# Kernel optimization log

Hardware: AMD Instinct MI355X
Metric: run time of the kernel (lower is better)

## Reference

```python
import jax, jax.numpy as jnp
import numpy as np

NEG_BIG = 1.0e10


def _strict_causal_mask(n):
    # mask[i, j] = 1.0 for j < i (strictly lower triangular), matching the
    # original loop `causal_mask[i, :i] = 1.0`.
    return jnp.tril(jnp.ones((n, n), dtype=jnp.float32), k=-1)


def setup_inputs() -> dict:
    rng = jax.random.key(0)
    k1, k2, k3 = jax.random.split(rng, 3)
    B, C, H, W = 8, 128, 64, 64
    return {
        "key": jax.random.normal(k1, (B, C, H, W), dtype=jnp.float32),
        "mixin": jax.random.normal(k2, (B, C, H, W), dtype=jnp.float32),
        "query": jax.random.normal(k3, (B, C, H, W), dtype=jnp.float32),
    }


def reference(key, mixin, query):
    B, Cq, H, W = query.shape
    Ck = key.shape[1]
    Cm = mixin.shape[1]
    N = H * W  # canvas_size

    # [B, C, H, W] -> [B, N, C]
    q = query.transpose(0, 2, 3, 1).reshape(B, N, Cq)
    k = key.transpose(0, 2, 3, 1).reshape(B, N, Ck)
    m = mixin.transpose(0, 2, 3, 1).reshape(B, N, Cm)

    mask = _strict_causal_mask(N)  # [N, N], broadcast over batch

    # raw scores with large-constant masking (matches original order of ops)
    dot = jnp.einsum("bqc,bkc->bqk", q, k) - (1.0 - mask) * NEG_BIG
    # NOTE: original subtracts the row max BEFORE scaling by 1/sqrt(d)
    dot = dot - jnp.max(dot, axis=-1, keepdims=True)
    causal_exp = jnp.exp(dot / jnp.sqrt(jnp.float32(Ck))) * mask
    probs = causal_exp / (jnp.sum(causal_exp, axis=-1, keepdims=True) + 1e-6)

    mixed = jnp.einsum("bqk,bkc->bqc", probs, m)  # [B, N, Cm]
    return mixed.reshape(B, H, W, Cm).transpose(0, 3, 1, 2)
```

## Files before the change

### kernel.cpp

```cpp
#include <hip/hip_runtime.h>
#include <hip/hip_bf16.h>
#include <stdint.h>


#define BATCH 8
#define CH    128
#define NN    4096
#define QBLK  64
#define KVBLK 64
#define C2 0.12751745f

typedef __attribute__((ext_vector_type(8))) short short8;
typedef __attribute__((ext_vector_type(16))) float f32x16;
typedef __attribute__((ext_vector_type(2))) int v2i;

__device__ __forceinline__ void gload16(const void* g, void* l) {
  __builtin_amdgcn_global_load_lds(
      (const __attribute__((address_space(1))) void*)g,
      (__attribute__((address_space(3))) void*)l, 16, 0, 0);
}

__device__ __forceinline__ int pk_bf16(float lo, float hi) {
  int d;
  asm("v_cvt_pk_bf16_f32 %0, %1, %2" : "=v"(d) : "v"(lo), "v"(hi));
  return d;
}

__device__ __forceinline__ void plswap(int& a, int& b) {
  v2i r = __builtin_amdgcn_permlane32_swap(a, b, false, false);
  a = r[0]; b = r[1];
}

__global__ __launch_bounds__(256) void prep_kernel(
    const float* __restrict__ key, const float* __restrict__ mixin,
    const float* __restrict__ query,
    unsigned short* __restrict__ qt, unsigned short* __restrict__ kt,
    unsigned short* __restrict__ vb) {
  int bid = blockIdx.x;
  int t = threadIdx.x;
  if (bid < 8192) {
    __shared__ float tl[32][33];
    const float* src = (bid < 4096) ? query : key;
    unsigned short* dst = (bid < 4096) ? qt : kt;
    int id = bid & 4095;
    int b = id >> 9;
    int tile = id & 511;
    int n0 = (tile >> 2) << 5;
    int c0 = (tile & 3) << 5;
    const float* sb = src + (size_t)b * CH * NN;
#pragma unroll
    for (int it = 0; it < 4; ++it) {
      int cl = it * 8 + (t >> 5);
      int nl = t & 31;
      tl[cl][nl] = sb[(size_t)(c0 + cl) * NN + n0 + nl];
    }
    __syncthreads();
    int nl = t >> 3;
    int cq = (t & 7) * 4;
    int d0 = pk_bf16(tl[cq + 0][nl], tl[cq + 1][nl]);
    int d1 = pk_bf16(tl[cq + 2][nl], tl[cq + 3][nl]);
    *(v2i*)&dst[(size_t)(b * NN + n0 + nl) * CH + c0 + cq] = (v2i){d0, d1};
  } else {
    int id = bid - 8192;
    size_t base = (size_t)id * 4096 + t * 4;
#pragma unroll
    for (int it = 0; it < 4; ++it) {
      size_t idx = base + (size_t)it * 1024;
      float4 v = *(const float4*)&mixin[idx];
      int d0 = pk_bf16(v.x, v.y);
      int d1 = pk_bf16(v.z, v.w);
      *(v2i*)&vb[idx] = (v2i){d0, d1};
    }
  }
}

__global__ __launch_bounds__(256, 2) void attn_kernel(
    const unsigned short* __restrict__ qt, const unsigned short* __restrict__ kt,
    const unsigned short* __restrict__ vb, float* __restrict__ out) {
  __shared__ __align__(16) unsigned char smem[65536];
  int tid = threadIdx.x;
  int wid = tid >> 6;
  int lane = tid & 63;
  int l31 = lane & 31;
  int hi = lane >> 5;
  int swz = (lane & 7) << 4;
  int qhalf = wid & 1;
  int h = wid >> 1;

  int gid = blockIdx.x;
  int b = gid & 7;
  int i = gid >> 3;
  int qb = (i < 32) ? (63 - i) : (i - 32);
  int q0 = qb * QBLK;
  int ntiles = qb + 1;

  const unsigned char* Qb = (const unsigned char*)(qt + (size_t)b * NN * CH);
  const unsigned char* Kb = (const unsigned char*)(kt + (size_t)b * NN * CH);
  const unsigned char* Vp = (const unsigned char*)(vb + (size_t)b * CH * NN);

  int kg[4], vg[4];
#pragma unroll
  for (int i2 = 0; i2 < 4; ++i2) {
    int row = wid * 16 + i2 * 4 + (lane >> 4);
    int slot = (lane & 15) ^ (row & 7);
    kg[i2] = row * 256 + slot * 16;
    int c = wid * 32 + i2 * 8 + (lane >> 3);
    int vslot = (lane & 7) ^ (c & 7);
    vg[i2] = c * 8192 + vslot * 16;
  }

#pragma unroll
  for (int i2 = 0; i2 < 4; ++i2) {
    gload16(Qb + (size_t)q0 * 256 + kg[i2], smem + 32768 + wid * 4096 + i2 * 1024);
    gload16(Kb + kg[i2], smem + wid * 4096 + i2 * 1024);
    gload16(Vp + vg[i2], smem + 16384 + wid * 4096 + i2 * 1024);
  }
  __syncthreads();

  short8 qf[8];
  {
    int qrb = 32768 + (qhalf * 32 + l31) * 256;
#pragma unroll
    for (int cs = 0; cs < 8; ++cs)
      qf[cs] = *(const short8*)&smem[qrb + ((cs * 32 + hi * 16) ^ swz)];
  }
  __syncthreads();

  f32x16 O[4];
#pragma unroll
  for (int ct = 0; ct < 4; ++ct)
#pragma unroll
    for (int r = 0; r < 16; ++r) O[ct][r] = 0.f;
  float m_run = -1e30f, l_run = 0.f;

  for (int t = 0; t < ntiles; ++t) {
    if (t + 1 < ntiles) {
      unsigned char* bk = smem + ((t + 1) & 1) * 32768;
      const unsigned char* Ks = Kb + (size_t)(t + 1) * 16384;
      const unsigned char* Vs = Vp + (size_t)(t + 1) * 128;
#pragma unroll
      for (int i2 = 0; i2 < 4; ++i2) {
        gload16(Ks + kg[i2], bk + wid * 4096 + i2 * 1024);
        gload16(Vs + vg[i2], bk + 16384 + wid * 4096 + i2 * 1024);
      }
    }
    if ((t & 1) == h) {
      const unsigned char* bk = smem + (t & 1) * 32768;
      const unsigned char* bv = bk + 16384;
      f32x16 S0, S1;
#pragma unroll
      for (int r = 0; r < 16; ++r) { S0[r] = 0.f; S1[r] = 0.f; }
#pragma unroll
      for (int cs = 0; cs < 8; ++cs) {
        int wo = (cs * 32 + hi * 16) ^ swz;
        short8 k0f = *(const short8*)&bk[l31 * 256 + wo];
        short8 k1f = *(const short8*)&bk[8192 + l31 * 256 + wo];
        S0 = __builtin_amdgcn_mfma_f32_32x32x16_bf16(k0f, qf[cs], S0, 0, 0, 0);
        S1 = __builtin_amdgcn_mfma_f32_32x32x16_bf16(k1f, qf[cs], S1, 0, 0, 0);
      }
      if (t == qb) {
        int ql = qhalf * 32 + l31;
#pragma unroll
        for (int r = 0; r < 16; ++r) {
          int kl = (r & 3) + 8 * (r >> 2) + 4 * hi;
          if (kl >= ql)      S0[r] = -__builtin_inff();
          if (kl + 32 >= ql) S1[r] = -__builtin_inff();
        }
      }
      float mx = S0[0];
#pragma unroll
      for (int r = 1; r < 16; ++r) mx = fmaxf(mx, S0[r]);
#pragma unroll
      for (int r = 0; r < 16; ++r) mx = fmaxf(mx, S1[r]);
      mx = fmaxf(mx, __shfl_xor(mx, 32));
      float mn = fmaxf(m_run, mx);
      float al = __builtin_amdgcn_exp2f((m_run - mn) * C2);
      m_run = mn;
      float rs = 0.f;
#pragma unroll
      for (int r = 0; r < 16; ++r) {
        S0[r] = __builtin_amdgcn_exp2f((S0[r] - mn) * C2);
        rs += S0[r];
      }
#pragma unroll
      for (int r = 0; r < 16; ++r) {
        S1[r] = __builtin_amdgcn_exp2f((S1[r] - mn) * C2);
        rs += S1[r];
      }
      rs += __shfl_xor(rs, 32);
      l_run = l_run * al + rs;
#pragma unroll
      for (int ct = 0; ct < 4; ++ct)
#pragma unroll
        for (int r = 0; r < 16; ++r) O[ct][r] *= al;
#pragma unroll
      for (int ks = 0; ks < 4; ++ks) {
        const f32x16& Sv = (ks >= 2) ? S1 : S0;
        int b8 = (ks & 1) * 8;
        int cA = pk_bf16(Sv[b8 + 0], Sv[b8 + 1]);
        int cB = pk_bf16(Sv[b8 + 2], Sv[b8 + 3]);
        int cC = pk_bf16(Sv[b8 + 4], Sv[b8 + 5]);
        int cD = pk_bf16(Sv[b8 + 6], Sv[b8 + 7]);
        plswap(cA, cC);
        plswap(cB, cD);
        union { int w[4]; short8 s; } pu;
        pu.w[0] = cA; pu.w[1] = cB; pu.w[2] = cC; pu.w[3] = cD;
        int vwo = (ks * 32 + hi * 16) ^ swz;
#pragma unroll
        for (int ct = 0; ct < 4; ++ct) {
          short8 vf = *(const short8*)&bv[(ct * 32 + l31) * 128 + vwo];
          O[ct] = __builtin_amdgcn_mfma_f32_32x32x16_bf16(vf, pu.s, O[ct], 0, 0, 0);
        }
      }
    }
    __syncthreads();
  }

  float* mlb = (float*)smem;
  float* ob = (float*)(smem + 4096);
  mlb[(wid * 64 + lane) * 2 + 0] = m_run;
  mlb[(wid * 64 + lane) * 2 + 1] = l_run;
  if (h == 1) {
#pragma unroll
    for (int ct = 0; ct < 4; ++ct)
#pragma unroll
      for (int r = 0; r < 16; ++r) {
        int c = ct * 32 + (r & 3) + 8 * (r >> 2) + 4 * hi;
        ob[c * 64 + qhalf * 32 + l31] = O[ct][r];
      }
  }
  __syncthreads();
  if (h == 0) {
    int pw = wid + 2;
    float m1 = mlb[(pw * 64 + lane) * 2 + 0];
    float l1 = mlb[(pw * 64 + lane) * 2 + 1];
    float ms = fmaxf(m_run, m1);
    float a0 = __builtin_amdgcn_exp2f((m_run - ms) * C2);
    float a1 = __builtin_amdgcn_exp2f((m1 - ms) * C2);
    float lt = l_run * a0 + l1 * a1;
    float rd = 1.0f / (lt + 1e-6f);
    int q = q0 + qhalf * 32 + l31;
#pragma unroll
    for (int ct = 0; ct < 4; ++ct)
#pragma unroll
      for (int r = 0; r < 16; ++r) {
        int c = ct * 32 + (r & 3) + 8 * (r >> 2) + 4 * hi;
        float v = (O[ct][r] * a0 + ob[c * 64 + qhalf * 32 + l31] * a1) * rd;
        out[(size_t)(b * CH + c) * NN + q] = v;
      }
  }
}

extern "C" void kernel_launch(void* const* d_in, const int* in_sizes, int n_in,
                              void* d_out, int out_size, void* d_ws, size_t ws_size,
                              hipStream_t stream) {
  const float* key = (const float*)d_in[0];
  const float* mixin = (const float*)d_in[1];
  const float* query = (const float*)d_in[2];
  float* out = (float*)d_out;

  unsigned short* qtp = (unsigned short*)d_ws;
  unsigned short* ktp = qtp + (size_t)BATCH * NN * CH;
  unsigned short* vbp = ktp + (size_t)BATCH * NN * CH;

  prep_kernel<<<9216, 256, 0, stream>>>(key, mixin, query, qtp, ktp, vbp);
  attn_kernel<<<512, 256, 0, stream>>>(qtp, ktp, vbp, out);
}
```

Measured before the change: 188.9 us.

## Shrink attention tiles to 32 and split KV tiles across four waves

The attention kernel now uses 32-row query and key/value tiles, 1024 blocks, and a smaller shared-memory footprint so four blocks can share a CU. Each of the four waves handles every fourth KV tile, and a tree reduction merges the partial results at the end. The change also skips the rescale when the running max grows by only a small amount, raises wave priority around MFMA sections, and rewrites the prep transpose to work on 64x128 tiles. More waves run concurrently and softmax work shrinks, at the cost of an extra merge stage and a rescale skip that could change numerics slightly.

```diff
diff --git a/kernel.cpp b/kernel.cpp
--- a/kernel.cpp
+++ b/kernel.cpp
@@ -6,11 +6,10 @@
 #define BATCH 8
 #define CH    128
 #define NN    4096
-#define QBLK  64
-#define KVBLK 64
 #define C2 0.12751745f
 
 typedef __attribute__((ext_vector_type(8))) short short8;
+typedef __attribute__((ext_vector_type(4))) float f32x4;
 typedef __attribute__((ext_vector_type(16))) float f32x16;
 typedef __attribute__((ext_vector_type(2))) int v2i;
 
@@ -37,92 +36,92 @@
     unsigned short* __restrict__ qt, unsigned short* __restrict__ kt,
     unsigned short* __restrict__ vb) {
   int bid = blockIdx.x;
-  int t = threadIdx.x;
-  if (bid < 8192) {
-    __shared__ float tl[32][33];
-    const float* src = (bid < 4096) ? query : key;
-    unsigned short* dst = (bid < 4096) ? qt : kt;
-    int id = bid & 4095;
-    int b = id >> 9;
-    int tile = id & 511;
-    int n0 = (tile >> 2) << 5;
-    int c0 = (tile & 3) << 5;
+  int tid = threadIdx.x;
+  if (bid < 1024) {
+    __shared__ float tlf[64 * 133];
+    const float* src = (bid < 512) ? query : key;
+    unsigned short* dst = (bid < 512) ? qt : kt;
+    int b = (bid >> 6) & 7;
+    int n0 = (bid & 63) * 64;
     const float* sb = src + (size_t)b * CH * NN;
-#pragma unroll
-    for (int it = 0; it < 4; ++it) {
-      int cl = it * 8 + (t >> 5);
-      int nl = t & 31;
-      tl[cl][nl] = sb[(size_t)(c0 + cl) * NN + n0 + nl];
+    int nl = (tid & 15) * 4;
+#pragma unroll
+    for (int i = 0; i < 8; ++i) {
+      int c = (tid >> 4) + i * 16;
+      float4 v = *(const float4*)&sb[(size_t)c * NN + n0 + nl];
+      tlf[(nl + 0) * 133 + c] = v.x;
+      tlf[(nl + 1) * 133 + c] = v.y;
+      tlf[(nl + 2) * 133 + c] = v.z;
+      tlf[(nl + 3) * 133 + c] = v.w;
     }
     __syncthreads();
-    int nl = t >> 3;
-    int cq = (t & 7) * 4;
-    int d0 = pk_bf16(tl[cq + 0][nl], tl[cq + 1][nl]);
-    int d1 = pk_bf16(tl[cq + 2][nl], tl[cq + 3][nl]);
-    *(v2i*)&dst[(size_t)(b * NN + n0 + nl) * CH + c0 + cq] = (v2i){d0, d1};
+    unsigned short* db = dst + (size_t)(b * NN + n0) * CH;
+    int c8 = (tid & 15) * 8;
+#pragma unroll
+    for (int i = 0; i < 4; ++i) {
+      int n = (tid >> 4) + i * 16;
+      const float* row = &tlf[n * 133 + c8];
+      int4 o;
+      o.x = pk_bf16(row[0], row[1]);
+      o.y = pk_bf16(row[2], row[3]);
+      o.z = pk_bf16(row[4], row[5]);
+      o.w = pk_bf16(row[6], row[7]);
+      *(int4*)&db[(size_t)n * CH + c8] = o;
+    }
   } else {
-    int id = bid - 8192;
-    size_t base = (size_t)id * 4096 + t * 4;
+    int id = bid - 1024;
+    size_t base = (size_t)id * 4096 + tid * 4;
 #pragma unroll
     for (int it = 0; it < 4; ++it) {
       size_t idx = base + (size_t)it * 1024;
       float4 v = *(const float4*)&mixin[idx];
-      int d0 = pk_bf16(v.x, v.y);
-      int d1 = pk_bf16(v.z, v.w);
-      *(v2i*)&vb[idx] = (v2i){d0, d1};
-    }
-  }
-}
-
-__global__ __launch_bounds__(256, 2) void attn_kernel(
+      v2i o;
+      o[0] = pk_bf16(v.x, v.y);
+      o[1] = pk_bf16(v.z, v.w);
+      *(v2i*)&vb[idx] = o;
+    }
+  }
+}
+
+__global__ __launch_bounds__(256, 4) void attn_kernel(
     const unsigned short* __restrict__ qt, const unsigned short* __restrict__ kt,
     const unsigned short* __restrict__ vb, float* __restrict__ out) {
-  __shared__ __align__(16) unsigned char smem[65536];
+  __shared__ __align__(16) unsigned char smem[35840];
   int tid = threadIdx.x;
   int wid = tid >> 6;
   int lane = tid & 63;
   int l31 = lane & 31;
   int hi = lane >> 5;
-  int swz = (lane & 7) << 4;
-  int qhalf = wid & 1;
-  int h = wid >> 1;
 
   int gid = blockIdx.x;
   int b = gid & 7;
   int i = gid >> 3;
-  int qb = (i < 32) ? (63 - i) : (i - 32);
-  int q0 = qb * QBLK;
+  int qb = (i < 64) ? (127 - i) : (i - 64);
+  int q0 = qb * 32;
   int ntiles = qb + 1;
 
   const unsigned char* Qb = (const unsigned char*)(qt + (size_t)b * NN * CH);
   const unsigned char* Kb = (const unsigned char*)(kt + (size_t)b * NN * CH);
   const unsigned char* Vp = (const unsigned char*)(vb + (size_t)b * CH * NN);
 
-  int kg[4], vg[4];
-#pragma unroll
-  for (int i2 = 0; i2 < 4; ++i2) {
-    int row = wid * 16 + i2 * 4 + (lane >> 4);
-    int slot = (lane & 15) ^ (row & 7);
-    kg[i2] = row * 256 + slot * 16;
-    int c = wid * 32 + i2 * 8 + (lane >> 3);
-    int vslot = (lane & 7) ^ (c & 7);
-    vg[i2] = c * 8192 + vslot * 16;
-  }
-
-#pragma unroll
-  for (int i2 = 0; i2 < 4; ++i2) {
-    gload16(Qb + (size_t)q0 * 256 + kg[i2], smem + 32768 + wid * 4096 + i2 * 1024);
-    gload16(Kb + kg[i2], smem + wid * 4096 + i2 * 1024);
-    gload16(Vp + vg[i2], smem + 16384 + wid * 4096 + i2 * 1024);
-  }
-  __syncthreads();
+  int kg[2], vg[2];
+#pragma unroll
+  for (int i2 = 0; i2 < 2; ++i2) {
+    int row = i2 * 16 + (tid >> 4);
+    kg[i2] = row * 256 + (((tid & 15) ^ (row & 7)) << 4);
+    int c = i2 * 64 + (tid >> 2);
+    vg[i2] = c * 8192 + (((tid & 3) ^ (c & 3)) << 4);
+  }
 
   short8 qf[8];
-  {
-    int qrb = 32768 + (qhalf * 32 + l31) * 256;
-#pragma unroll
-    for (int cs = 0; cs < 8; ++cs)
-      qf[cs] = *(const short8*)&smem[qrb + ((cs * 32 + hi * 16) ^ swz)];
+#pragma unroll
+  for (int cs = 0; cs < 8; ++cs)
+    qf[cs] = *(const short8*)&Qb[(size_t)(q0 + l31) * 256 + cs * 32 + hi * 16];
+
+#pragma unroll
+  for (int i2 = 0; i2 < 2; ++i2) {
+    gload16(Kb + kg[i2], smem + i2 * 4096 + tid * 16);
+    gload16(Vp + vg[i2], smem + 8192 + i2 * 4096 + tid * 16);
   }
   __syncthreads();
 
@@ -135,118 +134,153 @@
 
   for (int t = 0; t < ntiles; ++t) {
     if (t + 1 < ntiles) {
-      unsigned char* bk = smem + ((t + 1) & 1) * 32768;
-      const unsigned char* Ks = Kb + (size_t)(t + 1) * 16384;
-      const unsigned char* Vs = Vp + (size_t)(t + 1) * 128;
-#pragma unroll
-      for (int i2 = 0; i2 < 4; ++i2) {
-        gload16(Ks + kg[i2], bk + wid * 4096 + i2 * 1024);
-        gload16(Vs + vg[i2], bk + 16384 + wid * 4096 + i2 * 1024);
-      }
-    }
-    if ((t & 1) == h) {
-      const unsigned char* bk = smem + (t & 1) * 32768;
-      const unsigned char* bv = bk + 16384;
-      f32x16 S0, S1;
-#pragma unroll
-      for (int r = 0; r < 16; ++r) { S0[r] = 0.f; S1[r] = 0.f; }
+      unsigned char* nb = smem + ((t + 1) & 1) * 16384;
+      const unsigned char* Ks = Kb + (size_t)(t + 1) * 8192;
+      const unsigned char* Vs = Vp + (size_t)(t + 1) * 64;
+#pragma unroll
+      for (int i2 = 0; i2 < 2; ++i2) {
+        gload16(Ks + kg[i2], nb + i2 * 4096 + tid * 16);
+        gload16(Vs + vg[i2], nb + 8192 + i2 * 4096 + tid * 16);
+      }
+    }
+    if ((t & 3) == wid) {
+      const unsigned char* bk = smem + (t & 1) * 16384;
+      const unsigned char* bv = bk + 8192;
+      f32x16 S;
+#pragma unroll
+      for (int r = 0; r < 16; ++r) S[r] = 0.f;
+      __builtin_amdgcn_s_setprio(1);
 #pragma unroll
       for (int cs = 0; cs < 8; ++cs) {
-        int wo = (cs * 32 + hi * 16) ^ swz;
-        short8 k0f = *(const short8*)&bk[l31 * 256 + wo];
-        short8 k1f = *(const short8*)&bk[8192 + l31 * 256 + wo];
-        S0 = __builtin_amdgcn_mfma_f32_32x32x16_bf16(k0f, qf[cs], S0, 0, 0, 0);
-        S1 = __builtin_amdgcn_mfma_f32_32x32x16_bf16(k1f, qf[cs], S1, 0, 0, 0);
-      }
+        short8 kf = *(const short8*)&bk[l31 * 256 +
+                                        ((cs * 32 + hi * 16) ^ ((l31 & 7) << 4))];
+        S = __builtin_amdgcn_mfma_f32_32x32x16_bf16(kf, qf[cs], S, 0, 0, 0);
+      }
+      __builtin_amdgcn_s_setprio(0);
       if (t == qb) {
-        int ql = qhalf * 32 + l31;
 #pragma unroll
         for (int r = 0; r < 16; ++r) {
           int kl = (r & 3) + 8 * (r >> 2) + 4 * hi;
-          if (kl >= ql)      S0[r] = -__builtin_inff();
-          if (kl + 32 >= ql) S1[r] = -__builtin_inff();
+          if (kl >= l31) S[r] = -__builtin_inff();
         }
       }
-      float mx = S0[0];
-#pragma unroll
-      for (int r = 1; r < 16; ++r) mx = fmaxf(mx, S0[r]);
-#pragma unroll
-      for (int r = 0; r < 16; ++r) mx = fmaxf(mx, S1[r]);
+      float mx = S[0];
+#pragma unroll
+      for (int r = 1; r < 16; ++r) mx = fmaxf(mx, S[r]);
       mx = fmaxf(mx, __shfl_xor(mx, 32));
-      float mn = fmaxf(m_run, mx);
-      float al = __builtin_amdgcn_exp2f((m_run - mn) * C2);
-      m_run = mn;
+      bool skip = __all(mx - m_run <= 8.0f);
+      float mn, al;
+      if (skip) { mn = m_run; al = 1.0f; }
+      else { mn = fmaxf(m_run, mx); al = __builtin_amdgcn_exp2f((m_run - mn) * C2); m_run = mn; }
       float rs = 0.f;
 #pragma unroll
       for (int r = 0; r < 16; ++r) {
-        S0[r] = __builtin_amdgcn_exp2f((S0[r] - mn) * C2);
-        rs += S0[r];
-      }
-#pragma unroll
-      for (int r = 0; r < 16; ++r) {
-        S1[r] = __builtin_amdgcn_exp2f((S1[r] - mn) * C2);
-        rs += S1[r];
+        S[r] = __builtin_amdgcn_exp2f((S[r] - mn) * C2);
+        rs += S[r];
       }
       rs += __shfl_xor(rs, 32);
       l_run = l_run * al + rs;
-#pragma unroll
-      for (int ct = 0; ct < 4; ++ct)
-#pragma unroll
-        for (int r = 0; r < 16; ++r) O[ct][r] *= al;
-#pragma unroll
-      for (int ks = 0; ks < 4; ++ks) {
-        const f32x16& Sv = (ks >= 2) ? S1 : S0;
-        int b8 = (ks & 1) * 8;
-        int cA = pk_bf16(Sv[b8 + 0], Sv[b8 + 1]);
-        int cB = pk_bf16(Sv[b8 + 2], Sv[b8 + 3]);
-        int cC = pk_bf16(Sv[b8 + 4], Sv[b8 + 5]);
-        int cD = pk_bf16(Sv[b8 + 6], Sv[b8 + 7]);
+      if (!skip) {
+#pragma unroll
+        for (int ct = 0; ct < 4; ++ct)
+#pragma unroll
+          for (int r = 0; r < 16; ++r) O[ct][r] *= al;
+      }
+#pragma unroll
+      for (int ks = 0; ks < 2; ++ks) {
+        int b8 = ks * 8;
+        int cA = pk_bf16(S[b8 + 0], S[b8 + 1]);
+        int cB = pk_bf16(S[b8 + 2], S[b8 + 3]);
+        int cC = pk_bf16(S[b8 + 4], S[b8 + 5]);
+        int cD = pk_bf16(S[b8 + 6], S[b8 + 7]);
         plswap(cA, cC);
         plswap(cB, cD);
         union { int w[4]; short8 s; } pu;
         pu.w[0] = cA; pu.w[1] = cB; pu.w[2] = cC; pu.w[3] = cD;
-        int vwo = (ks * 32 + hi * 16) ^ swz;
+        int vwo = ks * 32 + hi * 16;
+        __builtin_amdgcn_s_setprio(1);
 #pragma unroll
         for (int ct = 0; ct < 4; ++ct) {
-          short8 vf = *(const short8*)&bv[(ct * 32 + l31) * 128 + vwo];
+          int c = ct * 32 + l31;
+          short8 vf = *(const short8*)&bv[c * 64 + (vwo ^ ((c & 3) << 4))];
           O[ct] = __builtin_amdgcn_mfma_f32_32x32x16_bf16(vf, pu.s, O[ct], 0, 0, 0);
         }
+        __builtin_amdgcn_s_setprio(0);
       }
     }
     __syncthreads();
   }
 
-  float* mlb = (float*)smem;
-  float* ob = (float*)(smem + 4096);
+  float* mlb = (float*)(smem + 33792);
+  unsigned char* regA = smem;
+  unsigned char* regB = smem + 16896;
   mlb[(wid * 64 + lane) * 2 + 0] = m_run;
   mlb[(wid * 64 + lane) * 2 + 1] = l_run;
-  if (h == 1) {
+  if (wid & 1) {
+    unsigned char* rg = (wid == 1) ? regA : regB;
 #pragma unroll
     for (int ct = 0; ct < 4; ++ct)
 #pragma unroll
-      for (int r = 0; r < 16; ++r) {
-        int c = ct * 32 + (r & 3) + 8 * (r >> 2) + 4 * hi;
-        ob[c * 64 + qhalf * 32 + l31] = O[ct][r];
+      for (int i4 = 0; i4 < 4; ++i4) {
+        f32x4 v = {O[ct][i4 * 4 + 0], O[ct][i4 * 4 + 1],
+                   O[ct][i4 * 4 + 2], O[ct][i4 * 4 + 3]};
+        *(f32x4*)&rg[lane * 264 + ct * 64 + i4 * 16] = v;
       }
   }
   __syncthreads();
-  if (h == 0) {
-    int pw = wid + 2;
-    float m1 = mlb[(pw * 64 + lane) * 2 + 0];
-    float l1 = mlb[(pw * 64 + lane) * 2 + 1];
+  if (!(wid & 1)) {
+    unsigned char* rg = (wid == 0) ? regA : regB;
+    int sw = wid + 1;
+    float m1 = mlb[(sw * 64 + lane) * 2 + 0];
+    float l1 = mlb[(sw * 64 + lane) * 2 + 1];
+    float ms = fmaxf(m_run, m1);
+    float a0 = __builtin_amdgcn_exp2f((m_run - ms) * C2);
+    float a1 = __builtin_amdgcn_exp2f((m1 - ms) * C2);
+#pragma unroll
+    for (int ct = 0; ct < 4; ++ct)
+#pragma unroll
+      for (int i4 = 0; i4 < 4; ++i4) {
+        f32x4 o1 = *(const f32x4*)&rg[lane * 264 + ct * 64 + i4 * 16];
+#pragma unroll
+        for (int j = 0; j < 4; ++j)
+          O[ct][i4 * 4 + j] = O[ct][i4 * 4 + j] * a0 + o1[j] * a1;
+      }
+    m_run = ms;
+    l_run = l_run * a0 + l1 * a1;
+  }
+  if (wid == 2) {
+#pragma unroll
+    for (int ct = 0; ct < 4; ++ct)
+#pragma unroll
+      for (int i4 = 0; i4 < 4; ++i4) {
+        f32x4 v = {O[ct][i4 * 4 + 0], O[ct][i4 * 4 + 1],
+                   O[ct][i4 * 4 + 2], O[ct][i4 * 4 + 3]};
+        *(f32x4*)&regB[lane * 264 + ct * 64 + i4 * 16] = v;
+      }
+    mlb[(2 * 64 + lane) * 2 + 0] = m_run;
+    mlb[(2 * 64 + lane) * 2 + 1] = l_run;
+  }
+  __syncthreads();
+  if (wid == 0) {
+    float m1 = mlb[(2 * 64 + lane) * 2 + 0];
+    float l1 = mlb[(2 * 64 + lane) * 2 + 1];
     float ms = fmaxf(m_run, m1);
     float a0 = __builtin_amdgcn_exp2f((m_run - ms) * C2);
     float a1 = __builtin_amdgcn_exp2f((m1 - ms) * C2);
     float lt = l_run * a0 + l1 * a1;
     float rd = 1.0f / (lt + 1e-6f);
-    int q = q0 + qhalf * 32 + l31;
+    int q = q0 + l31;
 #pragma unroll
     for (int ct = 0; ct < 4; ++ct)
 #pragma unroll
-      for (int r = 0; r < 16; ++r) {
-        int c = ct * 32 + (r & 3) + 8 * (r >> 2) + 4 * hi;
-        float v = (O[ct][r] * a0 + ob[c * 64 + qhalf * 32 + l31] * a1) * rd;
-        out[(size_t)(b * CH + c) * NN + q] = v;
+      for (int i4 = 0; i4 < 4; ++i4) {
+        f32x4 o1 = *(const f32x4*)&regB[lane * 264 + ct * 64 + i4 * 16];
+#pragma unroll
+        for (int j = 0; j < 4; ++j) {
+          int r = i4 * 4 + j;
+          int c = ct * 32 + (r & 3) + 8 * (r >> 2) + 4 * hi;
+          out[(size_t)(b * CH + c) * NN + q] = (O[ct][r] * a0 + o1[j] * a1) * rd;
+        }
       }
   }
 }
@@ -263,6 +297,6 @@
   unsigned short* ktp = qtp + (size_t)BATCH * NN * CH;
   unsigned short* vbp = ktp + (size_t)BATCH * NN * CH;
 
-  prep_kernel<<<9216, 256, 0, stream>>>(key, mixin, query, qtp, ktp, vbp);
-  attn_kernel<<<512, 256, 0, stream>>>(qtp, ktp, vbp, out);
-}
+  prep_kernel<<<2048, 256, 0, stream>>>(key, mixin, query, qtp, ktp, vbp);
+  attn_kernel<<<1024, 256, 0, stream>>>(qtp, ktp, vbp, out);
+}
```

Result: slower. 309.3 us (+63.8%).
